# Performance work log

Hardware: AMD Instinct MI355X
Metric: run time of the kernel (lower is better)

The kernel has to match this reference:

```python
import jax, jax.numpy as jnp
import numpy as np

# Module constants (kernels_desc / kernels_radius from the PA-Seg GatedCRF config)
RADIUS = (3, 3, 1)          # kernels_radius per (H, W, D)
SIGMA_XY = 5.0              # sigma for the spatial 'xy' mesh feature
SIGMA_IMG = 0.1             # sigma for the image intensity feature
WEIGHT = 1.0                # kernel weight


def _unfold(img, radius):
    """NCHWD -> (N, C, kH, kW, kD, H*W*D) sliding windows, zero-padded (matches unfoldNd)."""
    N, C, H, W, D = img.shape
    kH, kW, kD = (2 * radius[0] + 1, 2 * radius[1] + 1, 2 * radius[2] + 1)
    patches = jax.lax.conv_general_dilated_patches(
        img, (kH, kW, kD), (1, 1, 1),
        [(radius[0], radius[0]), (radius[1], radius[1]), (radius[2], radius[2])])
    # output channel dim is C-major over (C, kH, kW, kD)
    return patches.reshape(N, C, kH, kW, kD, H * W * D)


def _get_mesh(N, H, W, D, spacing, dtype):
    # spacing: (3, N) physical voxel spacings per axis per volume
    ah = jnp.arange(H, dtype=dtype)[None, :, None, None]
    aw = jnp.arange(W, dtype=dtype)[None, None, :, None]
    ad = jnp.arange(D, dtype=dtype)[None, None, None, :]
    sH = spacing[0][:, None, None, None]
    sW = spacing[1][:, None, None, None]
    sD = spacing[2][:, None, None, None]
    mh = jnp.broadcast_to(sH * ah, (N, H, W, D))
    mw = jnp.broadcast_to(sW * aw, (N, H, W, D))
    md = jnp.broadcast_to(sD * ad, (N, H, W, D))
    return jnp.stack([mh, mw, md], axis=1)  # (N, 3, H, W, D)


def _create_kernels(sample, spacing, N, H, W, D):
    mesh = _get_mesh(N, H, W, D, spacing, sample.dtype) / SIGMA_XY
    feats = jnp.concatenate([mesh, sample / SIGMA_IMG], axis=1)  # (N, 4, H, W, D)
    rH, rW, rD = RADIUS
    f_unf = _unfold(feats, RADIUS)                                # (N, 4, kH, kW, kD, L)
    center = f_unf[:, :, rH, rW, rD, :][:, :, None, None, None, :]
    k = jnp.exp((-0.5 * (f_unf - center) ** 2).sum(axis=1, keepdims=True))
    k = k.at[:, :, rH, rW, rD, :].set(0.0)
    return WEIGHT * k                                             # (N, 1, kH, kW, kD, L)


def setup_inputs() -> dict:
    key = jax.random.key(0)
    k1, k2, k3 = jax.random.split(key, 3)
    N, C, H, W, D = 1, 2, 64, 64, 32
    logits = jax.random.normal(k1, (N, C, H, W, D), dtype=jnp.float32)
    y_hat_softmax = jax.nn.softmax(logits, axis=1)
    sample = jax.random.normal(k2, (N, 1, H, W, D), dtype=jnp.float32)
    spacing = jax.random.uniform(k3, (3, N), dtype=jnp.float32, minval=0.5, maxval=2.0)
    return {"y_hat_softmax": y_hat_softmax, "sample": sample, "spacing": spacing}


def reference(y_hat_softmax, sample, spacing):
    N, C, H, W, D = y_hat_softmax.shape
    kernels = _create_kernels(sample, spacing, N, H, W, D)        # (N,1,kH,kW,kD,L)
    y_unf = _unfold(y_hat_softmax, RADIUS)                        # (N,C,kH,kW,kD,L)
    prod = (kernels * y_unf).sum(axis=(2, 3, 4))                  # (N, C, L)
    prod = prod.reshape(N, C, H, W, D)
    loss = kernels.sum() - (prod * y_hat_softmax).sum()
    denom = N * H * W * D
    return loss / denom
```

## Files before the change

### kernel.cpp

```cpp
#include <hip/hip_runtime.h>

#define NH 64
#define NW 64
#define ND 32
#define LTOT (NH * NW * ND)


__global__ __launch_bounds__(1024, 8)
void gatedcrf3d_kernel(const float* __restrict__ y,
                       const float* __restrict__ sample,
                       const float* __restrict__ spacing,
                       float* __restrict__ out)
{
    const int tid = threadIdx.x;
    const int sub = tid >> 7;
    const int v   = tid & 127;

    const int h = blockIdx.x >> 4;
    const int w = ((blockIdx.x & 15) << 2) + (v >> 5);
    const int d = v & 31;
    const int p = (h << 11) + (w << 5) + d;

    constexpr float L2E  = 1.4426950408889634f;
    constexpr float NHL2 = -0.5f * L2E;

    const float sH = spacing[0] * 0.2f;
    const float sW = spacing[1] * 0.2f;
    const float sD = spacing[2] * 0.2f;
    const float nh2 = NHL2 * sH * sH;
    const float nw2 = NHL2 * sW * sW;
    const float nd2 = NHL2 * sD * sD;

    const float ic  = sample[p] * 10.0f;
    const float y0c = y[p];
    const float y1c = y[LTOT + p];

    const int  zm = max(d - 1, 0);
    const int  zp = min(d + 1, ND - 1);
    const bool vm = d > 0;
    const bool vp = d < ND - 1;

    float acc = 0.0f, extra = 0.0f;

    auto PB = [&](int dh, int dw) {
        const int hh = h + dh;
        const int ww = w + dw;
        const bool ibhw = (hh < NH) & ((unsigned)ww < NW);
        const int hc = min(hh, NH - 1);
        const int wc = min(max(ww, 0), NW - 1);
        const int qb = (hc << 11) + (wc << 5);
        const float spat0 = nh2 * (float)(dh * dh) + nw2 * (float)(dw * dw);
        const float spat1 = spat0 + nd2;
        const int q0 = qb + zm, q1 = qb + d, q2 = qb + zp;
        const float s0 = sample[q0], s1 = sample[q1], s2 = sample[q2];
        const float a0 = y[q0],      a1 = y[q1],      a2 = y[q2];
        const float b0 = y[LTOT+q0], b1 = y[LTOT+q1], b2 = y[LTOT+q2];

        float di, arg, k, t;
        di  = __builtin_fmaf(s0, 10.0f, -ic);
        arg = __builtin_fmaf(di * NHL2, di, spat1);
        k   = __builtin_exp2f(arg);
        t   = 1.0f - __builtin_fmaf(a0, y0c, b0 * y1c);
        acc += (ibhw & vm) ? k * t : 0.0f;

        di  = __builtin_fmaf(s1, 10.0f, -ic);
        arg = __builtin_fmaf(di * NHL2, di, spat0);
        k   = __builtin_exp2f(arg);
        t   = 1.0f - __builtin_fmaf(a1, y0c, b1 * y1c);
        acc += ibhw ? k * t : 0.0f;

        di  = __builtin_fmaf(s2, 10.0f, -ic);
        arg = __builtin_fmaf(di * NHL2, di, spat1);
        k   = __builtin_exp2f(arg);
        t   = 1.0f - __builtin_fmaf(a2, y0c, b2 * y1c);
        acc += (ibhw & vp) ? k * t : 0.0f;
    };

    switch (sub) {
      case 0: PB(0,1); PB(0,2); PB(0,3); {
            const int q = (h << 11) + (w << 5) + zp;
            const float di  = __builtin_fmaf(sample[q], 10.0f, -ic);
            const float arg = __builtin_fmaf(di * NHL2, di, nd2);
            const float k   = __builtin_exp2f(arg);
            const float t   = 1.0f - __builtin_fmaf(y[q], y0c, y[LTOT + q] * y1c);
            acc += vp ? k * t : 0.0f;
        } break;
      case 1: PB(1,-3); PB(1,-2); PB(1,-1); break;
      case 2: PB(1, 0); PB(1, 1); PB(1, 2); break;
      case 3: PB(1, 3); PB(2,-3); PB(2,-2); break;
      case 4: PB(2,-1); PB(2, 0); PB(2, 1); break;
      case 5: PB(2, 2); PB(2, 3); PB(3,-3); break;
      case 6: PB(3,-2); PB(3,-1); PB(3, 0); break;
      case 7: PB(3, 1); PB(3, 2); PB(3, 3); {
            const int nhv = min(h, 3) + min(NH - 1 - h, 3) + 1;
            const int nwv = min(w, 3) + min(NW - 1 - w, 3) + 1;
            const int ndv = min(d, 1) + min(ND - 1 - d, 1) + 1;
            const int cnt = 147 - nhv * nwv * ndv;
            const float argo = nh2 * (float)(h * h) + nw2 * (float)(w * w)
                             + nd2 * (float)(d * d) + NHL2 * ic * ic;
            extra = (float)cnt * __builtin_exp2f(argo);
        } break;
    }

    float contrib = __builtin_fmaf(2.0f, acc, extra);

    #pragma unroll
    for (int off = 32; off > 0; off >>= 1)
        contrib += __shfl_down(contrib, off, 64);

    __shared__ float red[16];
    if ((tid & 63) == 0) red[tid >> 6] = contrib;
    __syncthreads();
    if (tid == 0) {
        float s = 0.0f;
        #pragma unroll
        for (int i = 0; i < 16; ++i) s += red[i];
        atomicAdd(out, s * (1.0f / (float)LTOT));
    }
}

extern "C" void kernel_launch(void* const* d_in, const int* in_sizes, int n_in,
                              void* d_out, int out_size, void* d_ws, size_t ws_size,
                              hipStream_t stream) {
    const float* y       = (const float*)d_in[0];
    const float* sample  = (const float*)d_in[1];
    const float* spacing = (const float*)d_in[2];
    float* out = (float*)d_out;

    hipMemsetAsync(out, 0, sizeof(float), stream);

    gatedcrf3d_kernel<<<LTOT / 128, 1024, 0, stream>>>(y, sample, spacing, out);
}
```

Before: 74.25 us.

## Process four depth voxels per thread with float4 loads and two-class simplification

Each thread now handles four consecutive depth positions and loads neighbour rows as float4 vectors plus two halo scalars, reusing each loaded row across three depth offsets. The two-class term is simplified using y1 = 1 - y0, so the second channel is no longer read. Work is redistributed into 12 block groups of 256 threads, each covering two neighbour offsets, instead of 8 sub-groups inside 1024-thread blocks. This cuts global load instructions and memory traffic per pair, at the cost of more registers per thread and fewer total threads. It also relies on the softmax inputs summing to one across the two channels.

```diff
diff --git a/kernel.cpp b/kernel.cpp
--- a/kernel.cpp
+++ b/kernel.cpp
@@ -6,20 +6,23 @@
 #define LTOT (NH * NW * ND)
 
 
-__global__ __launch_bounds__(1024, 8)
+__global__ __launch_bounds__(256, 8)
 void gatedcrf3d_kernel(const float* __restrict__ y,
                        const float* __restrict__ sample,
                        const float* __restrict__ spacing,
                        float* __restrict__ out)
 {
-    const int tid = threadIdx.x;
-    const int sub = tid >> 7;
-    const int v   = tid & 127;
+    const int tid   = threadIdx.x;
+    const int sub   = blockIdx.x >> 7;
+    const int group = ((blockIdx.x & 127) << 8) | tid;
+    const int h  = group >> 9;
+    const int w  = (group >> 3) & 63;
+    const int dg = group & 7;
+    const int d0 = dg << 2;
+    const int prow = (h << 11) + (w << 5);
 
-    const int h = blockIdx.x >> 4;
-    const int w = ((blockIdx.x & 15) << 2) + (v >> 5);
-    const int d = v & 31;
-    const int p = (h << 11) + (w << 5) + d;
+    const float4* __restrict__ s4p = (const float4*)sample;
+    const float4* __restrict__ y4p = (const float4*)y;
 
     constexpr float L2E  = 1.4426950408889634f;
     constexpr float NHL2 = -0.5f * L2E;
@@ -31,14 +34,12 @@
     const float nw2 = NHL2 * sW * sW;
     const float nd2 = NHL2 * sD * sD;
 
-    const float ic  = sample[p] * 10.0f;
-    const float y0c = y[p];
-    const float y1c = y[LTOT + p];
-
-    const int  zm = max(d - 1, 0);
-    const int  zp = min(d + 1, ND - 1);
-    const bool vm = d > 0;
-    const bool vp = d < ND - 1;
+    const float4 cs = s4p[(prow >> 2) + dg];
+    const float4 cy = y4p[(prow >> 2) + dg];
+    const float ic[4]  = {cs.x * 10.0f, cs.y * 10.0f, cs.z * 10.0f, cs.w * 10.0f};
+    const float yc[4]  = {cy.x, cy.y, cy.z, cy.w};
+    const float acv[4] = {__builtin_fmaf(-2.0f, cy.x, 1.0f), __builtin_fmaf(-2.0f, cy.y, 1.0f),
+                          __builtin_fmaf(-2.0f, cy.z, 1.0f), __builtin_fmaf(-2.0f, cy.w, 1.0f)};
 
     float acc = 0.0f, extra = 0.0f;
 
@@ -49,56 +50,78 @@
         const int hc = min(hh, NH - 1);
         const int wc = min(max(ww, 0), NW - 1);
         const int qb = (hc << 11) + (wc << 5);
+
+        float sv[6], yv[6];
+        const float4 fs = s4p[(qb >> 2) + dg];
+        const float4 fy = y4p[(qb >> 2) + dg];
+        sv[1] = fs.x; sv[2] = fs.y; sv[3] = fs.z; sv[4] = fs.w;
+        yv[1] = fy.x; yv[2] = fy.y; yv[3] = fy.z; yv[4] = fy.w;
+        const int im = qb + max(d0 - 1, 0);
+        const int ip = qb + min(d0 + 4, ND - 1);
+        sv[0] = sample[im]; sv[5] = sample[ip];
+        yv[0] = y[im];      yv[5] = y[ip];
+
         const float spat0 = nh2 * (float)(dh * dh) + nw2 * (float)(dw * dw);
         const float spat1 = spat0 + nd2;
-        const int q0 = qb + zm, q1 = qb + d, q2 = qb + zp;
-        const float s0 = sample[q0], s1 = sample[q1], s2 = sample[q2];
-        const float a0 = y[q0],      a1 = y[q1],      a2 = y[q2];
-        const float b0 = y[LTOT+q0], b1 = y[LTOT+q1], b2 = y[LTOT+q2];
 
-        float di, arg, k, t;
-        di  = __builtin_fmaf(s0, 10.0f, -ic);
-        arg = __builtin_fmaf(di * NHL2, di, spat1);
-        k   = __builtin_exp2f(arg);
-        t   = 1.0f - __builtin_fmaf(a0, y0c, b0 * y1c);
-        acc += (ibhw & vm) ? k * t : 0.0f;
-
-        di  = __builtin_fmaf(s1, 10.0f, -ic);
-        arg = __builtin_fmaf(di * NHL2, di, spat0);
-        k   = __builtin_exp2f(arg);
-        t   = 1.0f - __builtin_fmaf(a1, y0c, b1 * y1c);
-        acc += ibhw ? k * t : 0.0f;
-
-        di  = __builtin_fmaf(s2, 10.0f, -ic);
-        arg = __builtin_fmaf(di * NHL2, di, spat1);
-        k   = __builtin_exp2f(arg);
-        t   = 1.0f - __builtin_fmaf(a2, y0c, b2 * y1c);
-        acc += (ibhw & vp) ? k * t : 0.0f;
+        #pragma unroll
+        for (int j = 0; j < 4; ++j) {
+            #pragma unroll
+            for (int dd = -1; dd <= 1; ++dd) {
+                bool val = ibhw;
+                if (j == 0 && dd == -1) val = ibhw & (dg > 0);
+                if (j == 3 && dd ==  1) val = ibhw & (dg < 7);
+                const float sq = sv[1 + j + dd];
+                const float yq = yv[1 + j + dd];
+                const float di  = __builtin_fmaf(sq, 10.0f, -ic[j]);
+                const float arg = __builtin_fmaf(di * NHL2, di, dd ? spat1 : spat0);
+                const float k   = __builtin_exp2f(arg);
+                const float t   = __builtin_fmaf(yq, acv[j], yc[j]);
+                acc += val ? k * t : 0.0f;
+            }
+        }
     };
 
     switch (sub) {
-      case 0: PB(0,1); PB(0,2); PB(0,3); {
-            const int q = (h << 11) + (w << 5) + zp;
-            const float di  = __builtin_fmaf(sample[q], 10.0f, -ic);
-            const float arg = __builtin_fmaf(di * NHL2, di, nd2);
-            const float k   = __builtin_exp2f(arg);
-            const float t   = 1.0f - __builtin_fmaf(y[q], y0c, y[LTOT + q] * y1c);
-            acc += vp ? k * t : 0.0f;
+      case  0: PB(0, 1); PB(0, 2); {
+            const int ip = prow + min(d0 + 4, ND - 1);
+            const float s5 = sample[ip];
+            const float y5 = y[ip];
+            #pragma unroll
+            for (int j = 0; j < 4; ++j) {
+                const float di = (j < 3) ? (ic[j + 1] - ic[j])
+                                         : __builtin_fmaf(s5, 10.0f, -ic[3]);
+                const float yq = (j < 3) ? yc[j + 1] : y5;
+                const bool val = (j < 3) ? true : (dg < 7);
+                const float arg = __builtin_fmaf(di * NHL2, di, nd2);
+                const float k   = __builtin_exp2f(arg);
+                const float t   = __builtin_fmaf(yq, acv[j], yc[j]);
+                acc += val ? k * t : 0.0f;
+            }
         } break;
-      case 1: PB(1,-3); PB(1,-2); PB(1,-1); break;
-      case 2: PB(1, 0); PB(1, 1); PB(1, 2); break;
-      case 3: PB(1, 3); PB(2,-3); PB(2,-2); break;
-      case 4: PB(2,-1); PB(2, 0); PB(2, 1); break;
-      case 5: PB(2, 2); PB(2, 3); PB(3,-3); break;
-      case 6: PB(3,-2); PB(3,-1); PB(3, 0); break;
-      case 7: PB(3, 1); PB(3, 2); PB(3, 3); {
+      case  1: PB(0,  3); PB(1, -3); break;
+      case  2: PB(1, -2); PB(1, -1); break;
+      case  3: PB(1,  0); PB(1,  1); break;
+      case  4: PB(1,  2); PB(1,  3); break;
+      case  5: PB(2, -3); PB(2, -2); break;
+      case  6: PB(2, -1); PB(2,  0); break;
+      case  7: PB(2,  1); PB(2,  2); break;
+      case  8: PB(2,  3); PB(3, -3); break;
+      case  9: PB(3, -2); PB(3, -1); break;
+      case 10: PB(3,  0); PB(3,  1); break;
+      case 11: PB(3,  2); PB(3,  3); {
             const int nhv = min(h, 3) + min(NH - 1 - h, 3) + 1;
             const int nwv = min(w, 3) + min(NW - 1 - w, 3) + 1;
-            const int ndv = min(d, 1) + min(ND - 1 - d, 1) + 1;
-            const int cnt = 147 - nhv * nwv * ndv;
-            const float argo = nh2 * (float)(h * h) + nw2 * (float)(w * w)
-                             + nd2 * (float)(d * d) + NHL2 * ic * ic;
-            extra = (float)cnt * __builtin_exp2f(argo);
+            const float base = nh2 * (float)(h * h) + nw2 * (float)(w * w);
+            #pragma unroll
+            for (int j = 0; j < 4; ++j) {
+                const int dj  = d0 + j;
+                const int ndv = min(dj, 1) + min(ND - 1 - dj, 1) + 1;
+                const int cnt = 147 - nhv * nwv * ndv;
+                const float argo = __builtin_fmaf(nd2, (float)(dj * dj), base)
+                                 + NHL2 * ic[j] * ic[j];
+                extra += (float)cnt * __builtin_exp2f(argo);
+            }
         } break;
     }
 
@@ -108,14 +131,11 @@
     for (int off = 32; off > 0; off >>= 1)
         contrib += __shfl_down(contrib, off, 64);
 
-    __shared__ float red[16];
+    __shared__ float red[4];
     if ((tid & 63) == 0) red[tid >> 6] = contrib;
     __syncthreads();
     if (tid == 0) {
-        float s = 0.0f;
-        #pragma unroll
-        for (int i = 0; i < 16; ++i) s += red[i];
-        atomicAdd(out, s * (1.0f / (float)LTOT));
+        atomicAdd(out, (red[0] + red[1] + red[2] + red[3]) * (1.0f / (float)LTOT));
     }
 }
 
@@ -129,5 +149,5 @@
 
     hipMemsetAsync(out, 0, sizeof(float), stream);
 
-    gatedcrf3d_kernel<<<LTOT / 128, 1024, 0, stream>>>(y, sample, spacing, out);
+    gatedcrf3d_kernel<<<12 * 128, 256, 0, stream>>>(y, sample, spacing, out);
 }
```

Result: slower. 80.98 us (+9.1%).
